# Kernel tuning notes

Hardware: AMD Instinct MI355X
Metric: run time of the kernel (lower is better)

## Reference

```python
import jax, jax.numpy as jnp
import numpy as np

ALPHA = 0.5  # mixing weight between dot-product and wedge-norm terms


def setup_inputs() -> dict:
    key = jax.random.key(0)
    kq, kk, kv = jax.random.split(key, 3)
    B, L, H, E = 2, 2048, 8, 32
    queries = jax.random.normal(kq, (B, L, H, E), dtype=jnp.float32)
    keys = jax.random.normal(kk, (B, L, H, E), dtype=jnp.float32)
    values = jax.random.normal(kv, (B, L, H, E), dtype=jnp.float32)
    return {"queries": queries, "keys": keys, "values": values}


def reference(queries, keys, values):
    # queries: [B,L,H,E], keys: [B,S,H,E], values: [B,S,H,D]
    E = queries.shape[-1]
    scale = 1.0 / jnp.sqrt(jnp.asarray(E, dtype=queries.dtype))
    # dot product scores: [B,H,L,S]
    dot = jnp.einsum('blhe,bshe->bhls', queries, keys)
    # squared norms -> broadcastable [B,H,L,1] and [B,H,1,S]
    qn2 = jnp.sum(queries ** 2, axis=-1).transpose(0, 2, 1)[..., :, None]
    kn2 = jnp.sum(keys ** 2, axis=-1).transpose(0, 2, 1)[..., None, :]
    # wedge (Clifford) squared norm, clamped at 0
    wedge = jax.nn.relu(qn2 * kn2 - dot ** 2)
    scores = (ALPHA * dot - (1.0 - ALPHA) * wedge) * scale
    attn = jax.nn.softmax(scores, axis=-1)  # [B,H,L,S]
    # out: [B,L,H,D]
    out = jnp.einsum('bhls,bshd->blhd', attn, values)
    return out
```

## Files before the change

### kernel.cpp

```cpp
#include <hip/hip_runtime.h>
#include <hip/hip_bf16.h>
#include <math.h>


#define NB 2
#define NL 2048
#define NS 2048
#define NH 8
#define NBH 16
#define CSC 0.12751742f

#define WS_KN2_OFF 0u
#define WS_KHKL_OFF 131072u
#define WS_VT_OFF (131072u + 4194304u)
#define WS_PACC_OFF (131072u + 4194304u + 2097152u)
#define WS_PML_OFF (WS_PACC_OFF + 16777216u)
#define WS_NEED (WS_PML_OFF + 1048576u)

typedef float f32x4 __attribute__((ext_vector_type(4)));
typedef short s16x8 __attribute__((ext_vector_type(8)));
typedef unsigned short u16;

__device__ inline unsigned pk2(float a, float b) {
    __hip_bfloat162 t = __float22bfloat162_rn(make_float2(a, b));
    union { __hip_bfloat162 h; unsigned u; } cv;
    cv.h = t;
    return cv.u;
}
template <int CTRL>
__device__ inline float dpp_add(float x) {
    return x + __int_as_float(__builtin_amdgcn_mov_dpp(__float_as_int(x), CTRL, 0xF, 0xF, false));
}
__device__ inline void dma16(const void* gp, void* lp) {
    __builtin_amdgcn_global_load_lds(
        (__attribute__((address_space(1))) void*)(void*)gp,
        (__attribute__((address_space(3))) void*)lp, 16, 0, 0);
}
__device__ inline int swzK(int row) { return (row ^ (row >> 2)) & 3; }
__device__ inline int swzV(int row) { return (row + (row >> 3)) & 7; }

__global__ __launch_bounds__(256) void ga_pre(const float* __restrict__ K,
                                              const float* __restrict__ V,
                                              float* __restrict__ kn2w,
                                              u16* __restrict__ khkl,
                                              u16* __restrict__ vtw) {
    __shared__ float Vf[64][36];
    const int T = threadIdx.x;
    const int bh = blockIdx.x >> 5, stile = blockIdx.x & 31;
    const int b = bh >> 3, h = bh & 7;
    const int s0 = stile * 64;
    const int sk = T >> 2, kc = T & 3;

    const float* kp = K + ((size_t)((b * NS + s0 + sk) * NH + h)) * 32 + kc * 8;
    float4 f0 = *(const float4*)kp, f1 = *(const float4*)(kp + 4);
    float kx[8] = {f0.x, f0.y, f0.z, f0.w, f1.x, f1.y, f1.z, f1.w};
    unsigned hh[4], ll[4];
    float kn2p = 0.f;
#pragma unroll
    for (int i = 0; i < 4; i++) {
        float x0 = kx[2 * i], x1 = kx[2 * i + 1];
        kn2p = fmaf(x0, x0, kn2p);
        kn2p = fmaf(x1, x1, kn2p);
        unsigned h01 = pk2(x0, x1);
        hh[i] = h01;
        float h0 = __uint_as_float(h01 << 16);
        float h1 = __uint_as_float(h01 & 0xffff0000u);
        ll[i] = pk2(x0 - h0, x1 - h1);
    }
    u16* kd = khkl + ((size_t)(bh * NS + s0 + sk)) * 64;
    const int swk = sk & 7;
    *(uint4*)(kd + ((kc ^ swk) * 8)) = make_uint4(hh[0], hh[1], hh[2], hh[3]);
    *(uint4*)(kd + (((4 + kc) ^ swk) * 8)) = make_uint4(ll[0], ll[1], ll[2], ll[3]);
    kn2p = dpp_add<0xB1>(kn2p);
    kn2p = dpp_add<0x4E>(kn2p);
    if (kc == 0) kn2w[bh * NS + s0 + sk] = kn2p;

    const float* vp = V + ((size_t)((b * NS + s0 + sk) * NH + h)) * 32 + kc * 8;
    float4 g0 = *(const float4*)vp, g1 = *(const float4*)(vp + 4);
    *(float4*)&Vf[sk][kc * 8] = g0;
    *(float4*)&Vf[sk][kc * 8 + 4] = g1;
    __syncthreads();
    const int dr = T >> 3, c = T & 7;
    float vv[8];
#pragma unroll
    for (int i = 0; i < 8; i++) vv[i] = Vf[c * 8 + i][dr];
    const int phys = c ^ (dr & 7);
    *(uint4*)(vtw + ((size_t)(bh * 32 + dr)) * NS + s0 + phys * 8) =
        make_uint4(pk2(vv[0], vv[1]), pk2(vv[2], vv[3]), pk2(vv[4], vv[5]), pk2(vv[6], vv[7]));
}

__global__ __launch_bounds__(256, 3) void ga_pw(
    const float* __restrict__ Q, const float* __restrict__ kn2w,
    const u16* __restrict__ khkl, const u16* __restrict__ vtw,
    float* __restrict__ pacc, float* __restrict__ pml) {
    __shared__ union {
        struct {
            u16 K[4][32][64];
            u16 V[4][32][32];
            u16 P[4][64][32];
        } s;
        struct {
            float cacc[4][32][69];
            float2 cml[4][64];
        } c;
    } u;

    const int T = threadIdx.x;
    const int lane = T & 63, wave = T >> 6;
    const int g = lane >> 4, lc = lane & 15, g8 = g * 8;
    const int blk = blockIdx.x;
    const int qt = blk & 31, strip = (blk >> 5) & 3, bh = blk >> 7;
    const int b = bh >> 3, h = bh & 7;
    const int kw0 = strip * 512 + wave * 128;

    s16x8 qh[4], ql[4];
    float qn2[4];
#pragma unroll
    for (int qg = 0; qg < 4; qg++) {
        const float* qrow =
            Q + ((size_t)((b * NL + qt * 64 + 16 * qg + lc) * NH + h)) * 32 + g8;
        float4 qa = *(const float4*)qrow, qb = *(const float4*)(qrow + 4);
        float q8[8] = {qa.x, qa.y, qa.z, qa.w, qb.x, qb.y, qb.z, qb.w};
        union { unsigned u4[4]; s16x8 v; } H, L;
        float qp = 0.f;
#pragma unroll
        for (int i = 0; i < 4; i++) {
            float x0 = q8[2 * i], x1 = q8[2 * i + 1];
            qp = fmaf(x0, x0, qp);
            qp = fmaf(x1, x1, qp);
            unsigned h01 = pk2(x0, x1);
            H.u4[i] = h01;
            float h0 = __uint_as_float(h01 << 16);
            float h1 = __uint_as_float(h01 & 0xffff0000u);
            L.u4[i] = pk2(x0 - h0, x1 - h1);
        }
        qh[qg] = H.v;
        ql[qg] = L.v;
        qp += __shfl_xor(qp, 16);
        qp += __shfl_xor(qp, 32);
        qn2[qg] = qp;
    }

    const char* ksrcB =
        (const char*)khkl + ((size_t)(bh * NS + kw0)) * 128 + lane * 16;
    const int dL0 = lane >> 2, lu = lane & 3;
    const char* vpe[2];
    const char* vpo[2];
#pragma unroll
    for (int i = 0; i < 2; i++) {
        const int d = 16 * i + dL0, x = d & 7;
        const size_t rowb = ((size_t)(bh * 32 + d)) * NS + kw0;
        vpe[i] = (const char*)vtw + (rowb + (size_t)((lu ^ x) * 8)) * 2;
        vpo[i] = (const char*)vtw + (rowb + (size_t)((((4 + lu) ^ x)) * 8)) * 2;
    }
    const float* kn2b = kn2w + (size_t)bh * NS + kw0;

    float kmin;
    {
        f32x4 k0 = *(const f32x4*)(kn2b + 4 * g);
        f32x4 k1 = *(const f32x4*)(kn2b + 16 + 4 * g);
        float a = fminf(fminf(k0[0], k0[1]), fminf(k0[2], k0[3]));
        float bq = fminf(fminf(k1[0], k1[1]), fminf(k1[2], k1[3]));
        kmin = fminf(a, bq);
        kmin = fminf(kmin, __shfl_xor(kmin, 16));
        kmin = fminf(kmin, __shfl_xor(kmin, 32));
    }
    float m0[4], m0C[4];
#pragma unroll
    for (int qg = 0; qg < 4; qg++) {
        m0[qg] = -0.5f * qn2[qg] * kmin;
        m0C[qg] = -m0[qg] * CSC;
    }

#pragma unroll
    for (int i = 0; i < 4; i++) dma16(ksrcB + i * 1024, &u.s.K[wave][8 * i][0]);
    dma16(vpe[0], &u.s.V[wave][0][0]);
    dma16(vpe[1], &u.s.V[wave][16][0]);

    s16x8 ones;
#pragma unroll
    for (int i = 0; i < 8; i++) ones[i] = (short)0x3F80;

    f32x4 acc[2][4], lacc[4];
#pragma unroll
    for (int ds = 0; ds < 2; ds++)
#pragma unroll
        for (int qg = 0; qg < 4; qg++) acc[ds][qg] = (f32x4){0.f, 0.f, 0.f, 0.f};
#pragma unroll
    for (int qg = 0; qg < 4; qg++) lacc[qg] = (f32x4){0.f, 0.f, 0.f, 0.f};
    const f32x4 z = {0.f, 0.f, 0.f, 0.f};
    const int sw7 = lc & 7, sw3 = lc & 3;

    for (int t = 0; t < 4; ++t) {
        __builtin_amdgcn_s_waitcnt(0x0F70);

        f32x4 kn2v0 = *(const f32x4*)(kn2b + t * 32 + 4 * g);
        f32x4 kn2v1 = *(const f32x4*)(kn2b + t * 32 + 16 + 4 * g);

        s16x8 kh0 = *(s16x8*)&u.s.K[wave][lc][(g ^ sw7) * 8];
        s16x8 kl0 = *(s16x8*)&u.s.K[wave][lc][((4 + g) ^ sw7) * 8];
        s16x8 kh1 = *(s16x8*)&u.s.K[wave][16 + lc][(g ^ sw7) * 8];
        s16x8 kl1 = *(s16x8*)&u.s.K[wave][16 + lc][((4 + g) ^ sw7) * 8];
        s16x8 va0 = *(s16x8*)&u.s.V[wave][lc][g8];
        s16x8 va1 = *(s16x8*)&u.s.V[wave][16 + lc][g8];
        __builtin_amdgcn_s_waitcnt(0xC07F);

        if (t + 1 < 4) {
            const char* kB = ksrcB + (size_t)(t + 1) * 4096;
#pragma unroll
            for (int i = 0; i < 4; i++) dma16(kB + i * 1024, &u.s.K[wave][8 * i][0]);
            const char* v0 = (((t + 1) & 1) ? vpo[0] : vpe[0]) + ((t + 1) >> 1) * 128;
            const char* v1 = (((t + 1) & 1) ? vpo[1] : vpe[1]) + ((t + 1) >> 1) * 128;
            dma16(v0, &u.s.V[wave][0][0]);
            dma16(v1, &u.s.V[wave][16][0]);
        }

#pragma unroll
        for (int st = 0; st < 2; st++) {
            const s16x8 kh = st ? kh1 : kh0;
            const s16x8 kl = st ? kl1 : kl0;
            const f32x4 kn2v = st ? kn2v1 : kn2v0;
#pragma unroll
            for (int qg = 0; qg < 4; qg++) {
                f32x4 dd = __builtin_amdgcn_mfma_f32_16x16x32_bf16(kl, qh[qg], z, 0, 0, 0);
                dd = __builtin_amdgcn_mfma_f32_16x16x32_bf16(kh, ql[qg], dd, 0, 0, 0);
                dd = __builtin_amdgcn_mfma_f32_16x16x32_bf16(kh, qh[qg], dd, 0, 0, 0);
                float p[4];
#pragma unroll
                for (int r = 0; r < 4; r++) {
                    float dv = dd[r];
                    float c = qn2[qg] * kn2v[r];
                    float sc = fminf(dv, fmaf(dv, dv, -c) + dv);
                    p[r] = __builtin_amdgcn_exp2f(fmaf(sc, CSC, m0C[qg]));
                }
                const int phys = (2 * st + (g >> 1)) ^ sw3;
                *(uint2*)((char*)&u.s.P[wave][16 * qg + lc][0] + phys * 16 + (g & 1) * 8) =
                    make_uint2(pk2(p[0], p[1]), pk2(p[2], p[3]));
            }
        }
        __builtin_amdgcn_s_waitcnt(0xC07F);

#pragma unroll
        for (int qg = 0; qg < 4; qg++) {
            s16x8 pb = *(s16x8*)((char*)&u.s.P[wave][16 * qg + lc][0] + ((g ^ sw3) * 16));
            acc[0][qg] = __builtin_amdgcn_mfma_f32_16x16x32_bf16(va0, pb, acc[0][qg], 0, 0, 0);
            acc[1][qg] = __builtin_amdgcn_mfma_f32_16x16x32_bf16(va1, pb, acc[1][qg], 0, 0, 0);
            lacc[qg] = __builtin_amdgcn_mfma_f32_16x16x32_bf16(ones, pb, lacc[qg], 0, 0, 0);
        }
    }

    __syncthreads();
#pragma unroll
    for (int ds = 0; ds < 2; ds++)
#pragma unroll
        for (int qg = 0; qg < 4; qg++)
#pragma unroll
            for (int r = 0; r < 4; r++)
                u.c.cacc[wave][16 * ds + 4 * g + r][16 * qg + lc] = acc[ds][qg][r];
    if (g == 0) {
#pragma unroll
        for (int qg = 0; qg < 4; qg++)
            u.c.cml[wave][16 * qg + lc] = make_float2(m0[qg], lacc[qg][0]);
    }
    __syncthreads();

    const int q = T >> 2, dc = T & 3;
    float mm[4], llv[4];
#pragma unroll
    for (int w = 0; w < 4; w++) {
        float2 t2 = u.c.cml[w][q];
        mm[w] = t2.x;
        llv[w] = t2.y;
    }
    float mf = fmaxf(fmaxf(mm[0], mm[1]), fmaxf(mm[2], mm[3]));
    float e[4], L = 0.f;
#pragma unroll
    for (int w = 0; w < 4; w++) {
        e[w] = __builtin_amdgcn_exp2f((mm[w] - mf) * CSC);
        L = fmaf(llv[w], e[w], L);
    }
    float o[8];
#pragma unroll
    for (int i = 0; i < 8; i++) {
        const int d = dc * 8 + i;
        float s = 0.f;
#pragma unroll
        for (int w = 0; w < 4; w++) s = fmaf(u.c.cacc[w][d][q], e[w], s);
        o[i] = s;
    }
    float* pa = pacc + ((((size_t)bh * 4 + strip) * NL + qt * 64 + q)) * 32 + dc * 8;
    *(float4*)pa = make_float4(o[0], o[1], o[2], o[3]);
    *(float4*)(pa + 4) = make_float4(o[4], o[5], o[6], o[7]);
    if (dc == 0)
        *(float2*)(pml + (((size_t)bh * 4 + strip) * NL + qt * 64 + q) * 2) =
            make_float2(mf, L);
}

__global__ __launch_bounds__(256) void ga_combine(const float* __restrict__ pacc,
                                                  const float* __restrict__ pml,
                                                  float* __restrict__ O) {
    const int tid = blockIdx.x * 256 + threadIdx.x;
    const int dq = tid & 7, q = (tid >> 3) & 2047, bh = tid >> 14;
    const int b = bh >> 3, h = bh & 7;
    float m[4], l[4];
#pragma unroll
    for (int s = 0; s < 4; s++) {
        float2 t = *(const float2*)(pml + (((size_t)bh * 4 + s) * NL + q) * 2);
        m[s] = t.x;
        l[s] = t.y;
    }
    float mf = fmaxf(fmaxf(m[0], m[1]), fmaxf(m[2], m[3]));
    float w[4], L = 0.f;
#pragma unroll
    for (int s = 0; s < 4; s++) {
        w[s] = __builtin_amdgcn_exp2f((m[s] - mf) * CSC);
        L = fmaf(l[s], w[s], L);
    }
    const float inv = 1.f / L;
    float4 o = make_float4(0.f, 0.f, 0.f, 0.f);
#pragma unroll
    for (int s = 0; s < 4; s++) {
        const float* pa = pacc + (((size_t)bh * 4 + s) * NL + q) * 32 + dq * 4;
        float4 a = *(const float4*)pa;
        o.x = fmaf(a.x, w[s], o.x);
        o.y = fmaf(a.y, w[s], o.y);
        o.z = fmaf(a.z, w[s], o.z);
        o.w = fmaf(a.w, w[s], o.w);
    }
    o.x *= inv; o.y *= inv; o.z *= inv; o.w *= inv;
    *(float4*)(O + (((size_t)(b * NL + q)) * NH + h) * 32 + dq * 4) = o;
}

__global__ __launch_bounds__(512, 4) void ga_fallback(
    const float* __restrict__ Q, const float* __restrict__ K,
    const float* __restrict__ V, float* __restrict__ O) {
    __shared__ union {
        struct {
            u16 Kh[2][64][32];
            u16 Kl[2][64][32];
            u16 Vt[2][32][64];
            float kn2[2][64];
        } s;
        struct { float acc[8][32][17]; float m[8][16]; float l[8][16]; } c;
    } u;
    __shared__ u16 sP[8][16][64];

    const int T = threadIdx.x;
    const int lane = T & 63, wave = T >> 6;
    const int g = lane >> 4, lc = lane & 15, g8 = g * 8;
    const int half = wave >> 2;
    const int qt = blockIdx.x & 31;
    const int bh = blockIdx.x >> 5;
    const int b = bh >> 3, h = bh & 7;
    const int qw = qt * 64 + (wave & 3) * 16;

    const float* qrow = Q + ((size_t)((b * NL + qw + lc) * NH + h)) * 32 + g8;
    float4 qa = *(const float4*)qrow, qb = *(const float4*)(qrow + 4);
    float q8[8] = {qa.x, qa.y, qa.z, qa.w, qb.x, qb.y, qb.z, qb.w};
    union { unsigned u4[4]; s16x8 v; } qh_, ql_;
    float qn2 = 0.f;
#pragma unroll
    for (int i = 0; i < 4; i++) {
        float x0 = q8[2 * i], x1 = q8[2 * i + 1];
        qn2 = fmaf(x0, x0, qn2);
        qn2 = fmaf(x1, x1, qn2);
        unsigned h01 = pk2(x0, x1);
        qh_.u4[i] = h01;
        float h0 = __uint_as_float(h01 << 16);
        float h1 = __uint_as_float(h01 & 0xffff0000u);
        ql_.u4[i] = pk2(x0 - h0, x1 - h1);
    }
    const s16x8 qh = qh_.v, ql = ql_.v;
    qn2 += __shfl_xor(qn2, 16);
    qn2 += __shfl_xor(qn2, 32);

    const int Tl = T & 255;
    const int sk = Tl >> 2, kc = Tl & 3;
    const int dv = Tl & 31, vc = Tl >> 5;
    const float* kbase = K + ((size_t)(b * NS * NH) + h) * 32;
    const float* vbase = V + ((size_t)(b * NS * NH) + h) * 32;
    const int kphys = (kc ^ swzK(sk)) * 8;
    const int vphys = (vc ^ swzV(dv)) * 8;

    int s0 = half * 1024;
    float4 ka = *(const float4*)(kbase + (size_t)(s0 + sk) * 256 + kc * 8);
    float4 kb = *(const float4*)(kbase + (size_t)(s0 + sk) * 256 + kc * 8 + 4);
    float vr[8];
#pragma unroll
    for (int i = 0; i < 8; i++) vr[i] = vbase[(size_t)(s0 + 8 * vc + i) * 256 + dv];

    f32x4 acc0 = {0.f, 0.f, 0.f, 0.f}, acc1 = {0.f, 0.f, 0.f, 0.f};
    float m = -INFINITY, l = 0.f;

    for (int t = 0; t < 16; ++t) {
        {
            float kx[8] = {ka.x, ka.y, ka.z, ka.w, kb.x, kb.y, kb.z, kb.w};
            unsigned hh[4], ll[4];
            float kn2p = 0.f;
#pragma unroll
            for (int i = 0; i < 4; i++) {
                float x0 = kx[2 * i], x1 = kx[2 * i + 1];
                kn2p = fmaf(x0, x0, kn2p);
                kn2p = fmaf(x1, x1, kn2p);
                unsigned h01 = pk2(x0, x1);
                hh[i] = h01;
                float h0 = __uint_as_float(h01 << 16);
                float h1 = __uint_as_float(h01 & 0xffff0000u);
                ll[i] = pk2(x0 - h0, x1 - h1);
            }
            *(uint4*)&u.s.Kh[half][sk][kphys] = make_uint4(hh[0], hh[1], hh[2], hh[3]);
            *(uint4*)&u.s.Kl[half][sk][kphys] = make_uint4(ll[0], ll[1], ll[2], ll[3]);
            kn2p = dpp_add<0xB1>(kn2p);
            kn2p = dpp_add<0x4E>(kn2p);
            if (kc == 0) u.s.kn2[half][sk] = kn2p;
            *(uint4*)&u.s.Vt[half][dv][vphys] =
                make_uint4(pk2(vr[0], vr[1]), pk2(vr[2], vr[3]),
                           pk2(vr[4], vr[5]), pk2(vr[6], vr[7]));
        }
        const int tn = (t + 1 < 16) ? t + 1 : t;
        const int sn = half * 1024 + tn * 64;
        ka = *(const float4*)(kbase + (size_t)(sn + sk) * 256 + kc * 8);
        kb = *(const float4*)(kbase + (size_t)(sn + sk) * 256 + kc * 8 + 4);
#pragma unroll
        for (int i = 0; i < 8; i++) vr[i] = vbase[(size_t)(sn + 8 * vc + i) * 256 + dv];

        __syncthreads();

        f32x4 d[4], kn2v[4];
        const f32x4 z = {0.f, 0.f, 0.f, 0.f};
        const int skr = swzK(lc);
#pragma unroll
        for (int st = 0; st < 4; st++) {
            kn2v[st] = *(f32x4*)&u.s.kn2[half][16 * st + 4 * g];
            s16x8 kh = *(s16x8*)&u.s.Kh[half][16 * st + lc][(g ^ skr) * 8];
            s16x8 kl = *(s16x8*)&u.s.Kl[half][16 * st + lc][(g ^ skr) * 8];
            f32x4 dd = __builtin_amdgcn_mfma_f32_16x16x32_bf16(kl, qh, z, 0, 0, 0);
            dd = __builtin_amdgcn_mfma_f32_16x16x32_bf16(kh, ql, dd, 0, 0, 0);
            dd = __builtin_amdgcn_mfma_f32_16x16x32_bf16(kh, qh, dd, 0, 0, 0);
            d[st] = dd;
        }

        float sc[4][4];
#pragma unroll
        for (int st = 0; st < 4; st++)
#pragma unroll
            for (int r = 0; r < 4; r++) {
                float dd = d[st][r];
                float w = fmaxf(fmaf(-dd, dd, qn2 * kn2v[st][r]), 0.f);
                sc[st][r] = (dd - w) * CSC;
            }

        float x0 = fmaxf(fmaxf(sc[0][0], sc[0][1]), fmaxf(sc[0][2], sc[0][3]));
        float x1 = fmaxf(fmaxf(sc[1][0], sc[1][1]), fmaxf(sc[1][2], sc[1][3]));
        float x2 = fmaxf(fmaxf(sc[2][0], sc[2][1]), fmaxf(sc[2][2], sc[2][3]));
        float x3 = fmaxf(fmaxf(sc[3][0], sc[3][1]), fmaxf(sc[3][2], sc[3][3]));
        float tm = fmaxf(fmaxf(x0, x1), fmaxf(x2, x3));
        tm = fmaxf(tm, __shfl_xor(tm, 16));
        tm = fmaxf(tm, __shfl_xor(tm, 32));
        const float nm = fmaxf(m, tm);
        const float al = __builtin_amdgcn_exp2f(m - nm);
        m = nm;
        float p[4][4], ls = 0.f;
#pragma unroll
        for (int st = 0; st < 4; st++)
#pragma unroll
            for (int r = 0; r < 4; r++) {
                p[st][r] = __builtin_amdgcn_exp2f(sc[st][r] - nm);
                ls += p[st][r];
            }
        l = fmaf(l, al, ls);
        acc0 *= al;
        acc1 *= al;

#pragma unroll
        for (int st = 0; st < 4; st++) {
            const int off = ((2 * st + (g >> 1)) ^ (lc & 7)) * 8 + (g & 1) * 4;
            *(uint2*)&sP[wave][lc][off] =
                make_uint2(pk2(p[st][0], p[st][1]), pk2(p[st][2], p[st][3]));
        }
        __builtin_amdgcn_s_waitcnt(0xC07F);

        const int svl = swzV(lc), svh = swzV(lc + 16), spl = lc & 7;
        s16x8 va00 = *(s16x8*)&u.s.Vt[half][lc][(g ^ svl) * 8];
        s16x8 va01 = *(s16x8*)&u.s.Vt[half][lc][((4 + g) ^ svl) * 8];
        s16x8 va10 = *(s16x8*)&u.s.Vt[half][lc + 16][(g ^ svh) * 8];
        s16x8 va11 = *(s16x8*)&u.s.Vt[half][lc + 16][((4 + g) ^ svh) * 8];
        s16x8 pb0 = *(s16x8*)&sP[wave][lc][(g ^ spl) * 8];
        s16x8 pb1 = *(s16x8*)&sP[wave][lc][((4 + g) ^ spl) * 8];
        acc0 = __builtin_amdgcn_mfma_f32_16x16x32_bf16(va00, pb0, acc0, 0, 0, 0);
        acc0 = __builtin_amdgcn_mfma_f32_16x16x32_bf16(va01, pb1, acc0, 0, 0, 0);
        acc1 = __builtin_amdgcn_mfma_f32_16x16x32_bf16(va10, pb0, acc1, 0, 0, 0);
        acc1 = __builtin_amdgcn_mfma_f32_16x16x32_bf16(va11, pb1, acc1, 0, 0, 0);

        __syncthreads();
    }

    l += __shfl_xor(l, 16);
    l += __shfl_xor(l, 32);
#pragma unroll
    for (int r = 0; r < 4; r++) {
        u.c.acc[wave][4 * g + r][lc] = acc0[r];
        u.c.acc[wave][16 + 4 * g + r][lc] = acc1[r];
    }
    if (lane < 16) {
        u.c.m[wave][lc] = m;
        u.c.l[wave][lc] = l;
    }
    __syncthreads();

    const int q = T >> 3, dq = (T & 7) * 4, qr = q & 15;
    const int w0 = q >> 4, w1 = w0 + 4;
    float m0 = u.c.m[w0][qr], m1 = u.c.m[w1][qr];
    float l0 = u.c.l[w0][qr], l1 = u.c.l[w1][qr];
    float mf = fmaxf(m0, m1);
    float e0 = __builtin_amdgcn_exp2f(m0 - mf);
    float e1 = __builtin_amdgcn_exp2f(m1 - mf);
    float inv = 1.f / fmaf(l1, e1, l0 * e0);
    e0 *= inv;
    e1 *= inv;
    float4 o;
    o.x = u.c.acc[w0][dq + 0][qr] * e0 + u.c.acc[w1][dq + 0][qr] * e1;
    o.y = u.c.acc[w0][dq + 1][qr] * e0 + u.c.acc[w1][dq + 1][qr] * e1;
    o.z = u.c.acc[w0][dq + 2][qr] * e0 + u.c.acc[w1][dq + 2][qr] * e1;
    o.w = u.c.acc[w0][dq + 3][qr] * e0 + u.c.acc[w1][dq + 3][qr] * e1;
    *(float4*)(O + ((size_t)((b * NL + qt * 64 + q) * NH + h)) * 32 + dq) = o;
}

extern "C" void kernel_launch(void* const* d_in, const int* in_sizes, int n_in,
                              void* d_out, int out_size, void* d_ws, size_t ws_size,
                              hipStream_t stream) {
    const float* Q = (const float*)d_in[0];
    const float* K = (const float*)d_in[1];
    const float* V = (const float*)d_in[2];
    float* O = (float*)d_out;

    if (ws_size >= (size_t)WS_NEED) {
        float* kn2w = (float*)((char*)d_ws + WS_KN2_OFF);
        u16* khkl = (u16*)((char*)d_ws + WS_KHKL_OFF);
        u16* vtw = (u16*)((char*)d_ws + WS_VT_OFF);
        float* pacc = (float*)((char*)d_ws + WS_PACC_OFF);
        float* pml = (float*)((char*)d_ws + WS_PML_OFF);
        ga_pre<<<NBH * 32, 256, 0, stream>>>(K, V, kn2w, khkl, vtw);
        ga_pw<<<NBH * 32 * 4, 256, 0, stream>>>(Q, kn2w, khkl, vtw, pacc, pml);
        ga_combine<<<(NBH * NL * 8) / 256, 256, 0, stream>>>(pacc, pml, O);
    } else {
        ga_fallback<<<NBH * 32, 512, 0, stream>>>(Q, K, V, O);
    }
}
```

Measured before the change: 111.0 us.

## Keep softmax probabilities in registers by permuting V layout to match MFMA output

The V transpose in the preprocessing kernel now stores keys in a permuted order, so the score MFMA output fragments line up directly with the B-operand layout of the PV MFMA. Probabilities are packed into bf16 registers with a truncating byte-permute and fed straight into the accumulation, which removes the LDS P buffer, its stores and loads, and a wait. The smaller LDS footprint allows the occupancy hint to rise from 3 to 4 blocks. Packing by truncation instead of round-to-nearest slightly changes the numerics.

```diff
diff --git a/kernel.cpp b/kernel.cpp
--- a/kernel.cpp
+++ b/kernel.cpp
@@ -26,6 +26,9 @@
     union { __hip_bfloat162 h; unsigned u; } cv;
     cv.h = t;
     return cv.u;
+}
+__device__ inline unsigned pkt(float a, float b) {
+    return __builtin_amdgcn_perm(__float_as_uint(b), __float_as_uint(a), 0x07060302u);
 }
 template <int CTRL>
 __device__ inline float dpp_add(float x) {
@@ -80,16 +83,18 @@
     *(float4*)&Vf[sk][kc * 8] = g0;
     *(float4*)&Vf[sk][kc * 8 + 4] = g1;
     __syncthreads();
-    const int dr = T >> 3, c = T & 7;
+    const int uu = T & 3, sub = (T >> 2) & 1, dr = T >> 3;
     float vv[8];
 #pragma unroll
-    for (int i = 0; i < 8; i++) vv[i] = Vf[c * 8 + i][dr];
-    const int phys = c ^ (dr & 7);
-    *(uint4*)(vtw + ((size_t)(bh * 32 + dr)) * NS + s0 + phys * 8) =
+    for (int j = 0; j < 4; j++) vv[j] = Vf[sub * 32 + 4 * uu + j][dr];
+#pragma unroll
+    for (int j = 0; j < 4; j++) vv[4 + j] = Vf[sub * 32 + 16 + 4 * uu + j][dr];
+    const int phys = uu ^ ((dr >> 1) & 3);
+    *(uint4*)(vtw + ((size_t)(bh * 32 + dr)) * NS + s0 + sub * 32 + phys * 8) =
         make_uint4(pk2(vv[0], vv[1]), pk2(vv[2], vv[3]), pk2(vv[4], vv[5]), pk2(vv[6], vv[7]));
 }
 
-__global__ __launch_bounds__(256, 3) void ga_pw(
+__global__ __launch_bounds__(256, 4) void ga_reg(
     const float* __restrict__ Q, const float* __restrict__ kn2w,
     const u16* __restrict__ khkl, const u16* __restrict__ vtw,
     float* __restrict__ pacc, float* __restrict__ pml) {
@@ -97,7 +102,6 @@
         struct {
             u16 K[4][32][64];
             u16 V[4][32][32];
-            u16 P[4][64][32];
         } s;
         struct {
             float cacc[4][32][69];
@@ -141,18 +145,9 @@
         qn2[qg] = qp;
     }
 
-    const char* ksrcB =
-        (const char*)khkl + ((size_t)(bh * NS + kw0)) * 128 + lane * 16;
-    const int dL0 = lane >> 2, lu = lane & 3;
-    const char* vpe[2];
-    const char* vpo[2];
-#pragma unroll
-    for (int i = 0; i < 2; i++) {
-        const int d = 16 * i + dL0, x = d & 7;
-        const size_t rowb = ((size_t)(bh * 32 + d)) * NS + kw0;
-        vpe[i] = (const char*)vtw + (rowb + (size_t)((lu ^ x) * 8)) * 2;
-        vpo[i] = (const char*)vtw + (rowb + (size_t)((((4 + lu) ^ x)) * 8)) * 2;
-    }
+    const char* ksrcB = (const char*)khkl + ((size_t)(bh * NS + kw0)) * 128 + lane * 16;
+    const u16* vsrc0 = vtw + ((size_t)(bh * 32 + (lane >> 2))) * NS + kw0 + (lane & 3) * 8;
+    const u16* vsrc1 = vtw + ((size_t)(bh * 32 + 16 + (lane >> 2))) * NS + kw0 + (lane & 3) * 8;
     const float* kn2b = kn2w + (size_t)bh * NS + kw0;
 
     float kmin;
@@ -174,8 +169,8 @@
 
 #pragma unroll
     for (int i = 0; i < 4; i++) dma16(ksrcB + i * 1024, &u.s.K[wave][8 * i][0]);
-    dma16(vpe[0], &u.s.V[wave][0][0]);
-    dma16(vpe[1], &u.s.V[wave][16][0]);
+    dma16(vsrc0, &u.s.V[wave][0][0]);
+    dma16(vsrc1, &u.s.V[wave][16][0]);
 
     s16x8 ones;
 #pragma unroll
@@ -189,7 +184,7 @@
 #pragma unroll
     for (int qg = 0; qg < 4; qg++) lacc[qg] = (f32x4){0.f, 0.f, 0.f, 0.f};
     const f32x4 z = {0.f, 0.f, 0.f, 0.f};
-    const int sw7 = lc & 7, sw3 = lc & 3;
+    const int swK = lc & 7, swV = (lc >> 1) & 3;
 
     for (int t = 0; t < 4; ++t) {
         __builtin_amdgcn_s_waitcnt(0x0F70);
@@ -197,55 +192,56 @@
         f32x4 kn2v0 = *(const f32x4*)(kn2b + t * 32 + 4 * g);
         f32x4 kn2v1 = *(const f32x4*)(kn2b + t * 32 + 16 + 4 * g);
 
-        s16x8 kh0 = *(s16x8*)&u.s.K[wave][lc][(g ^ sw7) * 8];
-        s16x8 kl0 = *(s16x8*)&u.s.K[wave][lc][((4 + g) ^ sw7) * 8];
-        s16x8 kh1 = *(s16x8*)&u.s.K[wave][16 + lc][(g ^ sw7) * 8];
-        s16x8 kl1 = *(s16x8*)&u.s.K[wave][16 + lc][((4 + g) ^ sw7) * 8];
-        s16x8 va0 = *(s16x8*)&u.s.V[wave][lc][g8];
-        s16x8 va1 = *(s16x8*)&u.s.V[wave][16 + lc][g8];
+        s16x8 kh0 = *(s16x8*)&u.s.K[wave][lc][(g ^ swK) * 8];
+        s16x8 kl0 = *(s16x8*)&u.s.K[wave][lc][((4 + g) ^ swK) * 8];
+        s16x8 kh1 = *(s16x8*)&u.s.K[wave][16 + lc][(g ^ swK) * 8];
+        s16x8 kl1 = *(s16x8*)&u.s.K[wave][16 + lc][((4 + g) ^ swK) * 8];
+        s16x8 va0 = *(s16x8*)&u.s.V[wave][lc][(g ^ swV) * 8];
+        s16x8 va1 = *(s16x8*)&u.s.V[wave][16 + lc][(g ^ swV) * 8];
         __builtin_amdgcn_s_waitcnt(0xC07F);
 
         if (t + 1 < 4) {
             const char* kB = ksrcB + (size_t)(t + 1) * 4096;
 #pragma unroll
             for (int i = 0; i < 4; i++) dma16(kB + i * 1024, &u.s.K[wave][8 * i][0]);
-            const char* v0 = (((t + 1) & 1) ? vpo[0] : vpe[0]) + ((t + 1) >> 1) * 128;
-            const char* v1 = (((t + 1) & 1) ? vpo[1] : vpe[1]) + ((t + 1) >> 1) * 128;
-            dma16(v0, &u.s.V[wave][0][0]);
-            dma16(v1, &u.s.V[wave][16][0]);
-        }
-
-#pragma unroll
-        for (int st = 0; st < 2; st++) {
-            const s16x8 kh = st ? kh1 : kh0;
-            const s16x8 kl = st ? kl1 : kl0;
-            const f32x4 kn2v = st ? kn2v1 : kn2v0;
-#pragma unroll
-            for (int qg = 0; qg < 4; qg++) {
-                f32x4 dd = __builtin_amdgcn_mfma_f32_16x16x32_bf16(kl, qh[qg], z, 0, 0, 0);
-                dd = __builtin_amdgcn_mfma_f32_16x16x32_bf16(kh, ql[qg], dd, 0, 0, 0);
-                dd = __builtin_amdgcn_mfma_f32_16x16x32_bf16(kh, qh[qg], dd, 0, 0, 0);
-                float p[4];
-#pragma unroll
-                for (int r = 0; r < 4; r++) {
-                    float dv = dd[r];
-                    float c = qn2[qg] * kn2v[r];
-                    float sc = fminf(dv, fmaf(dv, dv, -c) + dv);
-                    p[r] = __builtin_amdgcn_exp2f(fmaf(sc, CSC, m0C[qg]));
-                }
-                const int phys = (2 * st + (g >> 1)) ^ sw3;
-                *(uint2*)((char*)&u.s.P[wave][16 * qg + lc][0] + phys * 16 + (g & 1) * 8) =
-                    make_uint2(pk2(p[0], p[1]), pk2(p[2], p[3]));
+            dma16(vsrc0 + (t + 1) * 32, &u.s.V[wave][0][0]);
+            dma16(vsrc1 + (t + 1) * 32, &u.s.V[wave][16][0]);
+        }
+
+        s16x8 pb[4];
+#pragma unroll
+        for (int qg = 0; qg < 4; qg++) {
+            f32x4 d0 = __builtin_amdgcn_mfma_f32_16x16x32_bf16(kl0, qh[qg], z, 0, 0, 0);
+            d0 = __builtin_amdgcn_mfma_f32_16x16x32_bf16(kh0, ql[qg], d0, 0, 0, 0);
+            d0 = __builtin_amdgcn_mfma_f32_16x16x32_bf16(kh0, qh[qg], d0, 0, 0, 0);
+            f32x4 d1 = __builtin_amdgcn_mfma_f32_16x16x32_bf16(kl1, qh[qg], z, 0, 0, 0);
+            d1 = __builtin_amdgcn_mfma_f32_16x16x32_bf16(kh1, ql[qg], d1, 0, 0, 0);
+            d1 = __builtin_amdgcn_mfma_f32_16x16x32_bf16(kh1, qh[qg], d1, 0, 0, 0);
+            float p0[4], p1[4];
+#pragma unroll
+            for (int r = 0; r < 4; r++) {
+                float dv = d0[r];
+                float c = qn2[qg] * kn2v0[r];
+                float sc = fminf(dv, fmaf(dv, dv, -c) + dv);
+                p0[r] = __builtin_amdgcn_exp2f(fmaf(sc, CSC, m0C[qg]));
+                dv = d1[r];
+                c = qn2[qg] * kn2v1[r];
+                sc = fminf(dv, fmaf(dv, dv, -c) + dv);
+                p1[r] = __builtin_amdgcn_exp2f(fmaf(sc, CSC, m0C[qg]));
             }
-        }
-        __builtin_amdgcn_s_waitcnt(0xC07F);
+            union { unsigned u4[4]; s16x8 v; } P;
+            P.u4[0] = pkt(p0[0], p0[1]);
+            P.u4[1] = pkt(p0[2], p0[3]);
+            P.u4[2] = pkt(p1[0], p1[1]);
+            P.u4[3] = pkt(p1[2], p1[3]);
+            pb[qg] = P.v;
+        }
 
 #pragma unroll
         for (int qg = 0; qg < 4; qg++) {
-            s16x8 pb = *(s16x8*)((char*)&u.s.P[wave][16 * qg + lc][0] + ((g ^ sw3) * 16));
-            acc[0][qg] = __builtin_amdgcn_mfma_f32_16x16x32_bf16(va0, pb, acc[0][qg], 0, 0, 0);
-            acc[1][qg] = __builtin_amdgcn_mfma_f32_16x16x32_bf16(va1, pb, acc[1][qg], 0, 0, 0);
-            lacc[qg] = __builtin_amdgcn_mfma_f32_16x16x32_bf16(ones, pb, lacc[qg], 0, 0, 0);
+            acc[0][qg] = __builtin_amdgcn_mfma_f32_16x16x32_bf16(va0, pb[qg], acc[0][qg], 0, 0, 0);
+            acc[1][qg] = __builtin_amdgcn_mfma_f32_16x16x32_bf16(va1, pb[qg], acc[1][qg], 0, 0, 0);
+            lacc[qg] = __builtin_amdgcn_mfma_f32_16x16x32_bf16(ones, pb[qg], lacc[qg], 0, 0, 0);
         }
     }
 
@@ -541,7 +537,7 @@
         float* pacc = (float*)((char*)d_ws + WS_PACC_OFF);
         float* pml = (float*)((char*)d_ws + WS_PML_OFF);
         ga_pre<<<NBH * 32, 256, 0, stream>>>(K, V, kn2w, khkl, vtw);
-        ga_pw<<<NBH * 32 * 4, 256, 0, stream>>>(Q, kn2w, khkl, vtw, pacc, pml);
+        ga_reg<<<NBH * 32 * 4, 256, 0, stream>>>(Q, kn2w, khkl, vtw, pacc, pml);
         ga_combine<<<(NBH * NL * 8) / 256, 256, 0, stream>>>(pacc, pml, O);
     } else {
         ga_fallback<<<NBH * 32, 512, 0, stream>>>(Q, K, V, O);
```

Measured after the change: 141.1 us. 27.1% more time.
